# Optimization experiments

Hardware: AMD Instinct MI355X
Metric: run time of the kernel (lower is better)

## Reference

```python
import jax, jax.numpy as jnp
import numpy as np

N_NODES = 100000
N_EDGES = 3200000
IN_FEAT = 512
HIDDEN = 64
N_GRAPHS = 2048


def setup_inputs() -> dict:
    key = jax.random.key(0)
    ks = jax.random.split(key, 8)
    x = jax.random.normal(ks[0], (N_NODES, IN_FEAT), dtype=jnp.float32)
    edge_index = jax.random.randint(ks[1], (2, N_EDGES), 0, N_NODES, dtype=jnp.int64)
    batch = jnp.sort(jax.random.randint(ks[2], (N_NODES,), 0, N_GRAPHS, dtype=jnp.int64))
    W1 = jax.random.normal(ks[3], (IN_FEAT, HIDDEN), dtype=jnp.float32) * (1.0 / np.sqrt(IN_FEAT))
    b1 = jnp.zeros((HIDDEN,), dtype=jnp.float32)
    W2 = jax.random.normal(ks[4], (HIDDEN, HIDDEN), dtype=jnp.float32) * (1.0 / np.sqrt(HIDDEN))
    b2 = jnp.zeros((HIDDEN,), dtype=jnp.float32)
    fc_w = jax.random.normal(ks[5], (HIDDEN, 1), dtype=jnp.float32) * (1.0 / np.sqrt(HIDDEN))
    fc_b = jnp.zeros((1,), dtype=jnp.float32)
    return {"x": x, "edge_index": edge_index, "batch": batch, "num_graphs": N_GRAPHS,
            "W1": W1, "b1": b1, "W2": W2, "b2": b2, "fc_w": fc_w, "fc_b": fc_b}


def _gcn_conv(x, src, dst, n_nodes, W, b):
    # PyG GCNConv: h = X W; out = D^{-1/2}(A+I)D^{-1/2} h + b  (self-loops already in src/dst)
    h = x @ W  # [N, out]
    ones = jnp.ones_like(src, dtype=h.dtype)
    deg = jax.ops.segment_sum(ones, dst, num_segments=n_nodes)  # in-degree incl. self-loop
    dinv = jnp.where(deg > 0, jax.lax.rsqrt(deg), 0.0)
    norm = dinv[src] * dinv[dst]  # [E+N]
    msgs = h[src] * norm[:, None]  # gather + scale
    out = jax.ops.segment_sum(msgs, dst, num_segments=n_nodes)  # scatter-add
    return out + b


def reference(x, edge_index, batch, num_graphs, W1, b1, W2, b2, fc_w, fc_b):
    n = x.shape[0]
    loops = jnp.arange(n, dtype=edge_index.dtype)
    src = jnp.concatenate([edge_index[0], loops])
    dst = jnp.concatenate([edge_index[1], loops])

    h = jax.nn.relu(_gcn_conv(x, src, dst, n, W1, b1))
    h = _gcn_conv(h, src, dst, n, W2, b2)

    # global_mean_pool over graph ids
    sums = jax.ops.segment_sum(h, batch, num_segments=num_graphs)
    cnts = jax.ops.segment_sum(jnp.ones((n,), dtype=h.dtype), batch, num_segments=num_graphs)
    pooled = sums / jnp.maximum(cnts, 1.0)[:, None]
    return pooled @ fc_w + fc_b  # [num_graphs, 1]
```

## Files before the change

kernel.cpp:

```cpp
#include <hip/hip_runtime.h>
#include <hip/hip_bf16.h>

#define N_NODES  100000
#define N_EDGES  3200000
#define IN_FEAT  512
#define HIDDEN   64
#define N_GRAPHS 2048
#define BSH      8
#define NPB      256
#define NBK      512
#define BCAP     10240
#define CH       4096

typedef __attribute__((ext_vector_type(8))) short short8;
typedef __attribute__((ext_vector_type(4))) float floatx4;

__device__ inline void bf16_split(float f, short& hi, short& lo) {
    unsigned u = __float_as_uint(f);
    unsigned r = (u + 0x7fffu + ((u >> 16) & 1u)) >> 16;
    float fh = __uint_as_float(r << 16);
    float fl = f - fh;
    unsigned v = __float_as_uint(fl);
    unsigned s = (v + 0x7fffu + ((v >> 16) & 1u)) >> 16;
    hi = (short)r;
    lo = (short)s;
}

__global__ __launch_bounds__(256) void fused_init(float* __restrict__ pooled,
                                                  int* __restrict__ cntg,
                                                  int* __restrict__ tail,
                                                  const int* __restrict__ batch,
                                                  const float* __restrict__ W1,
                                                  short* __restrict__ w1hi, short* __restrict__ w1lo,
                                                  const float* __restrict__ W2,
                                                  short* __restrict__ w2hi, short* __restrict__ w2lo,
                                                  int n, int g) {
    int i = blockIdx.x * 256 + threadIdx.x;
    if (i < g * 64) pooled[i] = 0.f;
    if (i < NBK) tail[i] = i * BCAP;
    if (i < IN_FEAT * 64) {
        int k = i >> 6, c = i & 63;
        short h, l;
        bf16_split(W1[i], h, l);
        w1hi[c * IN_FEAT + k] = h;
        w1lo[c * IN_FEAT + k] = l;
    }
    if (i < HIDDEN * 64) {
        int k = i >> 6, c = i & 63;
        short h, l;
        bf16_split(W2[i], h, l);
        w2hi[c * HIDDEN + k] = h;
        w2lo[c * HIDDEN + k] = l;
    }
    if (i < g) {
        int lo0 = 0, hi0 = n;
        while (lo0 < hi0) { int m = (lo0 + hi0) >> 1; if (batch[m] < i) lo0 = m + 1; else hi0 = m; }
        int lo1 = lo0, hi1 = n;
        while (lo1 < hi1) { int m = (lo1 + hi1) >> 1; if (batch[m] < i + 1) lo1 = m + 1; else hi1 = m; }
        cntg[i] = lo1 - lo0;
    }
}

__global__ __launch_bounds__(256) void bucket_scatter(const int* __restrict__ src,
                                                      const int* __restrict__ dst,
                                                      int* __restrict__ tail,
                                                      unsigned* __restrict__ packed, int e) {
    __shared__ int lcnt[NBK];
    __shared__ int sbase[NBK];
    int t = threadIdx.x;
    for (int b = t; b < NBK; b += 256) lcnt[b] = 0;
    __syncthreads();
    int base = blockIdx.x * CH;
    int bk[16]; int rk[16]; unsigned pk[16];
#pragma unroll
    for (int j = 0; j < 16; j++) {
        int idx = base + j * 256 + t;
        bk[j] = -1;
        if (idx < e) {
            int d = dst[idx], s = src[idx];
            bk[j] = d >> BSH;
            pk[j] = ((unsigned)(d & (NPB - 1)) << 17) | (unsigned)s;
            rk[j] = atomicAdd(&lcnt[bk[j]], 1);
        }
    }
    __syncthreads();
    for (int b = t; b < NBK; b += 256) {
        int c = lcnt[b];
        sbase[b] = c ? atomicAdd(&tail[b], c) : 0;
    }
    __syncthreads();
#pragma unroll
    for (int j = 0; j < 16; j++)
        if (bk[j] >= 0) {
            int slot = sbase[bk[j]] + rk[j];
            if (slot < (bk[j] + 1) * BCAP)
                packed[slot] = pk[j];
        }
}

__global__ void bucket_scan(const int* __restrict__ tail,
                            int* __restrict__ boff, int nb) {
    __shared__ int sA[512], sB[512];
    int t = threadIdx.x;
    int v = (t < nb) ? min(tail[t] - t * BCAP, BCAP) : 0;
    sA[t] = v;
    __syncthreads();
    int* pin = sA; int* pout = sB;
    for (int off = 1; off < 512; off <<= 1) {
        pout[t] = pin[t] + ((t >= off) ? pin[t - off] : 0);
        __syncthreads();
        int* tmp = pin; pin = pout; pout = tmp;
    }
    if (t < nb) boff[t] = pin[t] - v;
    if (t == 0) boff[nb] = pin[nb - 1];
}

__global__ __launch_bounds__(256) void bucket_csr(const unsigned* __restrict__ packed,
                                                  const int* __restrict__ boff,
                                                  int* __restrict__ csr,
                                                  int* __restrict__ row_start,
                                                  int* __restrict__ degi, int n) {
    __shared__ unsigned ed[BCAP];
    __shared__ int deg[NPB], excl[NPB], sA[NPB], sB[NPB];
    int b = blockIdx.x, t = threadIdx.x;
    int gbase = boff[b];
    int cnt = boff[b + 1] - gbase;
    if (cnt > BCAP) cnt = BCAP;
    const unsigned* pbase = packed + (size_t)b * BCAP;
    for (int i = t; i < cnt; i += 256) ed[i] = pbase[i];
    deg[t] = 0;
    __syncthreads();
    for (int i = t; i < cnt; i += 256) atomicAdd(&deg[ed[i] >> 17], 1);
    __syncthreads();
    sA[t] = deg[t];
    __syncthreads();
    int* pin = sA; int* pout = sB;
    for (int off = 1; off < NPB; off <<= 1) {
        pout[t] = pin[t] + ((t >= off) ? pin[t - off] : 0);
        __syncthreads();
        int* tmp = pin; pin = pout; pout = tmp;
    }
    excl[t] = pin[t] - deg[t];
    __syncthreads();
    int n0 = b << BSH;
    if (n0 + t < n) {
        row_start[n0 + t] = gbase + excl[t];
        degi[n0 + t] = deg[t] + 1;
    }
    __syncthreads();
    deg[t] = excl[t];
    __syncthreads();
    for (int i = t; i < cnt; i += 256) {
        unsigned p = ed[i];
        int d = p >> 17;
        int slot = atomicAdd(&deg[d], 1);
        csr[gbase + slot] = (int)(p & 0x1FFFFu);
    }
}

template <int K>
__global__ __launch_bounds__(256) void gemm_mfma(const float* __restrict__ X,
                                                 const short* __restrict__ Whi,
                                                 const short* __restrict__ Wlo,
                                                 const int* __restrict__ degi,
                                                 float* __restrict__ Y, int nrows) {
    const int t    = threadIdx.x;
    const int wave = t >> 6;
    const int lane = t & 63;
    const int quad = lane >> 4;
    const int l16  = lane & 15;

    const int arow   = blockIdx.x * 64 + wave * 16 + l16;
    const bool rvalid = arow < nrows;
    const float* xrow = X + (size_t)arow * K;

    floatx4 acc[4] = {};

#pragma unroll 1
    for (int k0 = 0; k0 < K; k0 += 32) {
        float av[8] = {0.f, 0.f, 0.f, 0.f, 0.f, 0.f, 0.f, 0.f};
        if (rvalid) {
            float4 p0 = *(const float4*)(xrow + k0 + quad * 8);
            float4 p1 = *(const float4*)(xrow + k0 + quad * 8 + 4);
            av[0] = p0.x; av[1] = p0.y; av[2] = p0.z; av[3] = p0.w;
            av[4] = p1.x; av[5] = p1.y; av[6] = p1.z; av[7] = p1.w;
        }
        short8 ahi, alo;
#pragma unroll
        for (int j = 0; j < 8; j++) { short h, l; bf16_split(av[j], h, l); ahi[j] = h; alo[j] = l; }

#pragma unroll
        for (int ct = 0; ct < 4; ct++) {
            int col = ct * 16 + l16;
            short8 bh = *(const short8*)(Whi + (size_t)col * K + k0 + quad * 8);
            short8 bl = *(const short8*)(Wlo + (size_t)col * K + k0 + quad * 8);
            acc[ct] = __builtin_amdgcn_mfma_f32_16x16x32_bf16(ahi, bh, acc[ct], 0, 0, 0);
            acc[ct] = __builtin_amdgcn_mfma_f32_16x16x32_bf16(ahi, bl, acc[ct], 0, 0, 0);
            acc[ct] = __builtin_amdgcn_mfma_f32_16x16x32_bf16(alo, bh, acc[ct], 0, 0, 0);
        }
    }

#pragma unroll
    for (int r = 0; r < 4; r++) {
        int orow = blockIdx.x * 64 + wave * 16 + quad * 4 + r;
        if (orow < nrows) {
            float dv = 1.0f / sqrtf((float)degi[orow]);
#pragma unroll
            for (int ct = 0; ct < 4; ct++)
                Y[(size_t)orow * 64 + ct * 16 + l16] = acc[ct][r] * dv;
        }
    }
}

template <bool RELU, bool POOL>
__global__ __launch_bounds__(256) void gcn_gather(const float* __restrict__ g,
                                                  const int* __restrict__ degi,
                                                  const int* __restrict__ row_start,
                                                  const int* __restrict__ csr_src,
                                                  const float* __restrict__ bias,
                                                  float* __restrict__ out,
                                                  float* __restrict__ pooled,
                                                  const int* __restrict__ batch, int n) {
    int node = (blockIdx.x * 256 + threadIdx.x) >> 6;
    int lane = threadIdx.x & 63;
    int es = lane >> 4;
    int fg = lane & 15;
    if (node >= n) return;

    int dg = degi[node];
    int de = dg - 1;
    float dn = 1.0f / sqrtf((float)dg);
    int start = row_start[node];

    float4 a0 = make_float4(0.f, 0.f, 0.f, 0.f);
    float4 a1 = a0, a2 = a0, a3 = a0;
    if (es == 0) a0 = *(const float4*)(g + (size_t)node * 64 + fg * 4);

    for (int c = 0; c < de; c += 64) {
        int m = min(64, de - c);
        int sv = (lane < m) ? csr_src[start + c + lane] : -1;
        int t = 0;
        for (; t + 16 <= m; t += 16) {
            int s0 = __shfl(sv, t + es);
            int s1 = __shfl(sv, t + 4 + es);
            int s2 = __shfl(sv, t + 8 + es);
            int s3 = __shfl(sv, t + 12 + es);
            float4 v0 = *(const float4*)(g + (size_t)s0 * 64 + fg * 4);
            float4 v1 = *(const float4*)(g + (size_t)s1 * 64 + fg * 4);
            float4 v2 = *(const float4*)(g + (size_t)s2 * 64 + fg * 4);
            float4 v3 = *(const float4*)(g + (size_t)s3 * 64 + fg * 4);
            a0.x += v0.x; a0.y += v0.y; a0.z += v0.z; a0.w += v0.w;
            a1.x += v1.x; a1.y += v1.y; a1.z += v1.z; a1.w += v1.w;
            a2.x += v2.x; a2.y += v2.y; a2.z += v2.z; a2.w += v2.w;
            a3.x += v3.x; a3.y += v3.y; a3.z += v3.z; a3.w += v3.w;
        }
        for (; t < m; t += 4) {
            int e = t + es;
            int s = __shfl(sv, e);
            if (e < m) {
                float4 v = *(const float4*)(g + (size_t)s * 64 + fg * 4);
                a0.x += v.x; a0.y += v.y; a0.z += v.z; a0.w += v.w;
            }
        }
    }
    float4 a;
    a.x = (a0.x + a1.x) + (a2.x + a3.x);
    a.y = (a0.y + a1.y) + (a2.y + a3.y);
    a.z = (a0.z + a1.z) + (a2.z + a3.z);
    a.w = (a0.w + a1.w) + (a2.w + a3.w);
    a.x += __shfl_xor(a.x, 16); a.y += __shfl_xor(a.y, 16);
    a.z += __shfl_xor(a.z, 16); a.w += __shfl_xor(a.w, 16);
    a.x += __shfl_xor(a.x, 32); a.y += __shfl_xor(a.y, 32);
    a.z += __shfl_xor(a.z, 32); a.w += __shfl_xor(a.w, 32);

    if (es == 0) {
        float4 bv = *(const float4*)(bias + fg * 4);
        float4 o;
        o.x = fmaf(dn, a.x, bv.x);
        o.y = fmaf(dn, a.y, bv.y);
        o.z = fmaf(dn, a.z, bv.z);
        o.w = fmaf(dn, a.w, bv.w);
        if (RELU) {
            o.x = fmaxf(o.x, 0.f); o.y = fmaxf(o.y, 0.f);
            o.z = fmaxf(o.z, 0.f); o.w = fmaxf(o.w, 0.f);
        }
        if (POOL) {
            float* pp = pooled + (size_t)batch[node] * 64 + fg * 4;
            atomicAdd(pp + 0, o.x);
            atomicAdd(pp + 1, o.y);
            atomicAdd(pp + 2, o.z);
            atomicAdd(pp + 3, o.w);
        } else {
            *(float4*)(out + (size_t)node * 64 + fg * 4) = o;
        }
    }
}

__global__ __launch_bounds__(256) void final_fc(const float* __restrict__ pooled,
                                                const int* __restrict__ cntg,
                                                const float* __restrict__ fc_w,
                                                const float* __restrict__ fc_b,
                                                float* __restrict__ out, int g) {
    int gid = (blockIdx.x * 256 + threadIdx.x) >> 6;
    int lane = threadIdx.x & 63;
    if (gid >= g) return;
    float c = fmaxf((float)cntg[gid], 1.0f);
    float v = pooled[(size_t)gid * 64 + lane] / c * fc_w[lane];
#pragma unroll
    for (int off = 32; off > 0; off >>= 1) v += __shfl_down(v, off);
    if (lane == 0) out[gid] = v + fc_b[0];
}

extern "C" void kernel_launch(void* const* d_in, const int* in_sizes, int n_in,
                              void* d_out, int out_size, void* d_ws, size_t ws_size,
                              hipStream_t stream) {
    const float* x    = (const float*)d_in[0];
    const int*   eidx = (const int*)d_in[1];
    const int*   batch= (const int*)d_in[2];
    const float* W1   = (const float*)d_in[4];
    const float* b1   = (const float*)d_in[5];
    const float* W2   = (const float*)d_in[6];
    const float* b2   = (const float*)d_in[7];
    const float* fc_w = (const float*)d_in[8];
    const float* fc_b = (const float*)d_in[9];
    float* out = (float*)d_out;

    const int N = in_sizes[0] / IN_FEAT;
    const int E = in_sizes[1] / 2;
    const int G = N_GRAPHS;
    const int* src = eidx;
    const int* dst = eidx + E;
    const int nb = (N + NPB - 1) >> BSH;

    char* w = (char*)d_ws;
    float* g1   = (float*)w; w += (size_t)N * 64 * 4;
    float* h1r  = (float*)w; w += (size_t)N * 64 * 4;
    float* g2   = (float*)w; w += (size_t)N * 64 * 4;
    int*   degi = (int*)w;   w += (size_t)N * 4;
    int*   rowst= (int*)w;   w += (size_t)N * 4;
    int*   boff = (int*)w;   w += (NBK + 1) * 4 + 12;
    int*   tail = (int*)w;   w += NBK * 4;
    unsigned* packed = (unsigned*)w; w += (size_t)NBK * BCAP * 4;
    int*   csrs = (int*)w;   w += (size_t)E * 4;
    float* pooled = (float*)w; w += (size_t)G * 64 * 4;
    int*   cntg = (int*)w;   w += (size_t)G * 4;
    short* w1hi = (short*)w; w += (size_t)IN_FEAT * 64 * 2;
    short* w1lo = (short*)w; w += (size_t)IN_FEAT * 64 * 2;
    short* w2hi = (short*)w; w += (size_t)HIDDEN * 64 * 2;
    short* w2lo = (short*)w; w += (size_t)HIDDEN * 64 * 2;

    fused_init<<<512, 256, 0, stream>>>(pooled, cntg, tail, batch,
                                        W1, w1hi, w1lo, W2, w2hi, w2lo, N, G);
    bucket_scatter<<<(E + CH - 1) / CH, 256, 0, stream>>>(src, dst, tail, packed, E);
    bucket_scan<<<1, 512, 0, stream>>>(tail, boff, nb);
    bucket_csr<<<nb, 256, 0, stream>>>(packed, boff, csrs, rowst, degi, N);

    gemm_mfma<IN_FEAT><<<(N + 63) / 64, 256, 0, stream>>>(x, w1hi, w1lo, degi, g1, N);
    gcn_gather<true, false><<<(N * 64 + 255) / 256, 256, 0, stream>>>(
        g1, degi, rowst, csrs, b1, h1r, nullptr, batch, N);
    gemm_mfma<HIDDEN><<<(N + 63) / 64, 256, 0, stream>>>(h1r, w2hi, w2lo, degi, g2, N);
    gcn_gather<false, true><<<(N * 64 + 255) / 256, 256, 0, stream>>>(
        g2, degi, rowst, csrs, b2, nullptr, pooled, batch, N);
    final_fc<<<(G * 64 + 255) / 256, 256, 0, stream>>>(pooled, cntg, fc_w, fc_b, out, G);
}
```

Baseline: 731.8 us.

## Store layer-1 features in bf16 and fuse second GEMM into first gather

The first GEMM now writes its degree-scaled output as bf16, which halves the bytes read by the random-access neighbour gather. The layer-1 gather kernel then applies bias and ReLU and multiplies by W2 in registers using shuffles and FMA. This removes the h1 intermediate buffer, the second GEMM launch and the W2 bf16 split. The risks are precision loss from bf16 storage of the layer-1 features and extra per-node FMA and shuffle work inside the gather.

```diff
diff --git a/kernel.cpp b/kernel.cpp
--- a/kernel.cpp
+++ b/kernel.cpp
@@ -26,14 +26,21 @@
     lo = (short)s;
 }
 
+__device__ inline unsigned short bf16_rne(float f) {
+    unsigned u = __float_as_uint(f);
+    return (unsigned short)((u + 0x7fffu + ((u >> 16) & 1u)) >> 16);
+}
+
+__device__ inline float bf16_f32(unsigned short v) {
+    return __uint_as_float(((unsigned)v) << 16);
+}
+
 __global__ __launch_bounds__(256) void fused_init(float* __restrict__ pooled,
                                                   int* __restrict__ cntg,
                                                   int* __restrict__ tail,
                                                   const int* __restrict__ batch,
                                                   const float* __restrict__ W1,
                                                   short* __restrict__ w1hi, short* __restrict__ w1lo,
-                                                  const float* __restrict__ W2,
-                                                  short* __restrict__ w2hi, short* __restrict__ w2lo,
                                                   int n, int g) {
     int i = blockIdx.x * 256 + threadIdx.x;
     if (i < g * 64) pooled[i] = 0.f;
@@ -44,13 +51,6 @@
         bf16_split(W1[i], h, l);
         w1hi[c * IN_FEAT + k] = h;
         w1lo[c * IN_FEAT + k] = l;
-    }
-    if (i < HIDDEN * 64) {
-        int k = i >> 6, c = i & 63;
-        short h, l;
-        bf16_split(W2[i], h, l);
-        w2hi[c * HIDDEN + k] = h;
-        w2lo[c * HIDDEN + k] = l;
     }
     if (i < g) {
         int lo0 = 0, hi0 = n;
@@ -163,7 +163,7 @@
                                                  const short* __restrict__ Whi,
                                                  const short* __restrict__ Wlo,
                                                  const int* __restrict__ degi,
-                                                 float* __restrict__ Y, int nrows) {
+                                                 unsigned short* __restrict__ Yb, int nrows) {
     const int t    = threadIdx.x;
     const int wave = t >> 6;
     const int lane = t & 63;
@@ -207,20 +207,106 @@
             float dv = 1.0f / sqrtf((float)degi[orow]);
 #pragma unroll
             for (int ct = 0; ct < 4; ct++)
-                Y[(size_t)orow * 64 + ct * 16 + l16] = acc[ct][r] * dv;
-        }
-    }
-}
-
-template <bool RELU, bool POOL>
-__global__ __launch_bounds__(256) void gcn_gather(const float* __restrict__ g,
-                                                  const int* __restrict__ degi,
-                                                  const int* __restrict__ row_start,
-                                                  const int* __restrict__ csr_src,
-                                                  const float* __restrict__ bias,
-                                                  float* __restrict__ out,
-                                                  float* __restrict__ pooled,
-                                                  const int* __restrict__ batch, int n) {
+                Yb[(size_t)orow * 64 + ct * 16 + l16] = bf16_rne(acc[ct][r] * dv);
+        }
+    }
+}
+
+__global__ __launch_bounds__(256) void gcn_gather_fuse(const unsigned short* __restrict__ g1b,
+                                                       const int* __restrict__ degi,
+                                                       const int* __restrict__ row_start,
+                                                       const int* __restrict__ csr_src,
+                                                       const float* __restrict__ b1,
+                                                       const float* __restrict__ W2,
+                                                       float* __restrict__ g2, int n) {
+    int node = (blockIdx.x * 256 + threadIdx.x) >> 6;
+    int lane = threadIdx.x & 63;
+    int es = lane >> 4;
+    int fg = lane & 15;
+    if (node >= n) return;
+
+    int dg = degi[node];
+    int de = dg - 1;
+    float dn = 1.0f / sqrtf((float)dg);
+    int start = row_start[node];
+
+    float4 a0 = make_float4(0.f, 0.f, 0.f, 0.f);
+    float4 a1 = a0, a2 = a0, a3 = a0;
+    if (es == 0) {
+        ushort4 v = *(const ushort4*)(g1b + (size_t)node * 64 + fg * 4);
+        a0.x = bf16_f32(v.x); a0.y = bf16_f32(v.y);
+        a0.z = bf16_f32(v.z); a0.w = bf16_f32(v.w);
+    }
+
+    for (int c = 0; c < de; c += 64) {
+        int m = min(64, de - c);
+        int sv = (lane < m) ? csr_src[start + c + lane] : -1;
+        int t = 0;
+        for (; t + 16 <= m; t += 16) {
+            int s0 = __shfl(sv, t + es);
+            int s1 = __shfl(sv, t + 4 + es);
+            int s2 = __shfl(sv, t + 8 + es);
+            int s3 = __shfl(sv, t + 12 + es);
+            ushort4 v0 = *(const ushort4*)(g1b + (size_t)s0 * 64 + fg * 4);
+            ushort4 v1 = *(const ushort4*)(g1b + (size_t)s1 * 64 + fg * 4);
+            ushort4 v2 = *(const ushort4*)(g1b + (size_t)s2 * 64 + fg * 4);
+            ushort4 v3 = *(const ushort4*)(g1b + (size_t)s3 * 64 + fg * 4);
+            a0.x += bf16_f32(v0.x); a0.y += bf16_f32(v0.y); a0.z += bf16_f32(v0.z); a0.w += bf16_f32(v0.w);
+            a1.x += bf16_f32(v1.x); a1.y += bf16_f32(v1.y); a1.z += bf16_f32(v1.z); a1.w += bf16_f32(v1.w);
+            a2.x += bf16_f32(v2.x); a2.y += bf16_f32(v2.y); a2.z += bf16_f32(v2.z); a2.w += bf16_f32(v2.w);
+            a3.x += bf16_f32(v3.x); a3.y += bf16_f32(v3.y); a3.z += bf16_f32(v3.z); a3.w += bf16_f32(v3.w);
+        }
+        for (; t < m; t += 4) {
+            int e = t + es;
+            int s = __shfl(sv, e);
+            if (e < m) {
+                ushort4 v = *(const ushort4*)(g1b + (size_t)s * 64 + fg * 4);
+                a0.x += bf16_f32(v.x); a0.y += bf16_f32(v.y);
+                a0.z += bf16_f32(v.z); a0.w += bf16_f32(v.w);
+            }
+        }
+    }
+    float4 a;
+    a.x = (a0.x + a1.x) + (a2.x + a3.x);
+    a.y = (a0.y + a1.y) + (a2.y + a3.y);
+    a.z = (a0.z + a1.z) + (a2.z + a3.z);
+    a.w = (a0.w + a1.w) + (a2.w + a3.w);
+    a.x += __shfl_xor(a.x, 16); a.y += __shfl_xor(a.y, 16);
+    a.z += __shfl_xor(a.z, 16); a.w += __shfl_xor(a.w, 16);
+    a.x += __shfl_xor(a.x, 32); a.y += __shfl_xor(a.y, 32);
+    a.z += __shfl_xor(a.z, 32); a.w += __shfl_xor(a.w, 32);
+
+    float4 bv = *(const float4*)(b1 + fg * 4);
+    float4 o;
+    o.x = fmaxf(fmaf(dn, a.x, bv.x), 0.f);
+    o.y = fmaxf(fmaf(dn, a.y, bv.y), 0.f);
+    o.z = fmaxf(fmaf(dn, a.z, bv.z), 0.f);
+    o.w = fmaxf(fmaf(dn, a.w, bv.w), 0.f);
+
+    float acc2 = 0.f;
+#pragma unroll
+    for (int fgj = 0; fgj < 16; fgj++) {
+        float4 ov;
+        ov.x = __shfl(o.x, fgj);
+        ov.y = __shfl(o.y, fgj);
+        ov.z = __shfl(o.z, fgj);
+        ov.w = __shfl(o.w, fgj);
+        const float* wr = W2 + (size_t)(fgj * 4) * 64 + lane;
+        acc2 = fmaf(ov.x, wr[0],   acc2);
+        acc2 = fmaf(ov.y, wr[64],  acc2);
+        acc2 = fmaf(ov.z, wr[128], acc2);
+        acc2 = fmaf(ov.w, wr[192], acc2);
+    }
+    g2[(size_t)node * 64 + lane] = dn * acc2;
+}
+
+__global__ __launch_bounds__(256) void gcn_gather_pool(const float* __restrict__ g,
+                                                       const int* __restrict__ degi,
+                                                       const int* __restrict__ row_start,
+                                                       const int* __restrict__ csr_src,
+                                                       const float* __restrict__ bias,
+                                                       float* __restrict__ pooled,
+                                                       const int* __restrict__ batch, int n) {
     int node = (blockIdx.x * 256 + threadIdx.x) >> 6;
     int lane = threadIdx.x & 63;
     int es = lane >> 4;
@@ -280,19 +366,11 @@
         o.y = fmaf(dn, a.y, bv.y);
         o.z = fmaf(dn, a.z, bv.z);
         o.w = fmaf(dn, a.w, bv.w);
-        if (RELU) {
-            o.x = fmaxf(o.x, 0.f); o.y = fmaxf(o.y, 0.f);
-            o.z = fmaxf(o.z, 0.f); o.w = fmaxf(o.w, 0.f);
-        }
-        if (POOL) {
-            float* pp = pooled + (size_t)batch[node] * 64 + fg * 4;
-            atomicAdd(pp + 0, o.x);
-            atomicAdd(pp + 1, o.y);
-            atomicAdd(pp + 2, o.z);
-            atomicAdd(pp + 3, o.w);
-        } else {
-            *(float4*)(out + (size_t)node * 64 + fg * 4) = o;
-        }
+        float* pp = pooled + (size_t)batch[node] * 64 + fg * 4;
+        atomicAdd(pp + 0, o.x);
+        atomicAdd(pp + 1, o.y);
+        atomicAdd(pp + 2, o.z);
+        atomicAdd(pp + 3, o.w);
     }
 }
 
@@ -333,8 +411,7 @@
     const int nb = (N + NPB - 1) >> BSH;
 
     char* w = (char*)d_ws;
-    float* g1   = (float*)w; w += (size_t)N * 64 * 4;
-    float* h1r  = (float*)w; w += (size_t)N * 64 * 4;
+    unsigned short* g1b = (unsigned short*)w; w += (size_t)N * 64 * 2;
     float* g2   = (float*)w; w += (size_t)N * 64 * 4;
     int*   degi = (int*)w;   w += (size_t)N * 4;
     int*   rowst= (int*)w;   w += (size_t)N * 4;
@@ -346,20 +423,16 @@
     int*   cntg = (int*)w;   w += (size_t)G * 4;
     short* w1hi = (short*)w; w += (size_t)IN_FEAT * 64 * 2;
     short* w1lo = (short*)w; w += (size_t)IN_FEAT * 64 * 2;
-    short* w2hi = (short*)w; w += (size_t)HIDDEN * 64 * 2;
-    short* w2lo = (short*)w; w += (size_t)HIDDEN * 64 * 2;
-
-    fused_init<<<512, 256, 0, stream>>>(pooled, cntg, tail, batch,
-                                        W1, w1hi, w1lo, W2, w2hi, w2lo, N, G);
+
+    fused_init<<<512, 256, 0, stream>>>(pooled, cntg, tail, batch, W1, w1hi, w1lo, N, G);
     bucket_scatter<<<(E + CH - 1) / CH, 256, 0, stream>>>(src, dst, tail, packed, E);
     bucket_scan<<<1, 512, 0, stream>>>(tail, boff, nb);
     bucket_csr<<<nb, 256, 0, stream>>>(packed, boff, csrs, rowst, degi, N);
 
-    gemm_mfma<IN_FEAT><<<(N + 63) / 64, 256, 0, stream>>>(x, w1hi, w1lo, degi, g1, N);
-    gcn_gather<true, false><<<(N * 64 + 255) / 256, 256, 0, stream>>>(
-        g1, degi, rowst, csrs, b1, h1r, nullptr, batch, N);
-    gemm_mfma<HIDDEN><<<(N + 63) / 64, 256, 0, stream>>>(h1r, w2hi, w2lo, degi, g2, N);
-    gcn_gather<false, true><<<(N * 64 + 255) / 256, 256, 0, stream>>>(
-        g2, degi, rowst, csrs, b2, nullptr, pooled, batch, N);
+    gemm_mfma<IN_FEAT><<<(N + 63) / 64, 256, 0, stream>>>(x, w1hi, w1lo, degi, g1b, N);
+    gcn_gather_fuse<<<(N * 64 + 255) / 256, 256, 0, stream>>>(
+        g1b, degi, rowst, csrs, b1, W2, g2, N);
+    gcn_gather_pool<<<(N * 64 + 255) / 256, 256, 0, stream>>>(
+        g2, degi, rowst, csrs, b2, pooled, batch, N);
     final_fc<<<(G * 64 + 255) / 256, 256, 0, stream>>>(pooled, cntg, fc_w, fc_b, out, G);
 }
```

After: 702.6 us. -4.0%, faster.
